# Kernel optimization log

Hardware: AMD Instinct MI355X
Metric: run time of the kernel (lower is better)

Reference implementation:

```python
import jax, jax.numpy as jnp
import numpy as np

N_HEADS = 16
ROPE_BASE = 10000.0


def rope_cos_sin(seq_len, dim, base=ROPE_BASE):
    inv_freq = 1.0 / (base ** (jnp.arange(0, dim, 2, dtype=jnp.float32) / dim))
    t = jnp.arange(seq_len, dtype=jnp.float32)
    freqs = jnp.outer(t, inv_freq)              # (S, dim/2)
    emb = jnp.concatenate([freqs, freqs], -1)   # (S, dim)
    return jnp.cos(emb), jnp.sin(emb)


def rotate_half(x):
    half = x.shape[-1] // 2
    return jnp.concatenate([-x[..., half:], x[..., :half]], axis=-1)


def setup_inputs() -> dict:
    key = jax.random.key(0)
    ks = jax.random.split(key, 6)
    B, S, D, DL, DKV = 2, 2048, 2048, 512, 2048
    s = 0.02
    return {
        "hidden_states": jax.random.normal(ks[0], (B, S, D), jnp.float32),
        "Wq": jax.random.normal(ks[1], (N_HEADS * 128, D), jnp.float32) * s,
        "Wc": jax.random.normal(ks[2], (DL, D), jnp.float32) * s,
        "Wk": jax.random.normal(ks[3], (DKV, DL), jnp.float32) * s,
        "Wv": jax.random.normal(ks[4], (DKV, DL), jnp.float32) * s,
        "Wo": jax.random.normal(ks[5], (D, N_HEADS * 128), jnp.float32) * s,
    }


def reference(hidden_states, Wq, Wc, Wk, Wv, Wo):
    B, S, D = hidden_states.shape
    H = N_HEADS
    DH = Wq.shape[0] // H

    # Q projection
    q = (hidden_states @ Wq.T).reshape(B, S, H, DH).transpose(0, 2, 1, 3)  # (B,H,S,DH)
    # latent KV compression + decompression
    c_kv = hidden_states @ Wc.T                                            # (B,S,DL)
    k = (c_kv @ Wk.T).reshape(B, S, H, DH).transpose(0, 2, 1, 3)
    v = (c_kv @ Wv.T).reshape(B, S, H, DH).transpose(0, 2, 1, 3)

    # RoPE (positions 0..S-1 for both q and k; no cache)
    cos, sin = rope_cos_sin(S, DH)
    cos = cos[None, None].astype(q.dtype)
    sin = sin[None, None].astype(q.dtype)
    q = q * cos + rotate_half(q) * sin
    k = k * cos + rotate_half(k) * sin

    scale = 1.0 / np.sqrt(DH).astype(np.float32)
    scores = jnp.einsum('bhqd,bhkd->bhqk', q, k) * scale
    causal = jnp.where(jnp.arange(S)[None, :] > jnp.arange(S)[:, None],
                       jnp.float32(-jnp.inf), jnp.float32(0.0))
    scores = scores + causal[None, None].astype(scores.dtype)
    attn = jax.nn.softmax(scores.astype(jnp.float32), axis=-1).astype(q.dtype)
    out = jnp.einsum('bhqk,bhkd->bhqd', attn, v)
    out = out.transpose(0, 2, 1, 3).reshape(B, S, H * DH)
    return out @ Wo.T
```

## Files before the change

### kernel.cpp

```cpp
#include <hip/hip_runtime.h>
#include <hip/hip_bf16.h>
#include <stdint.h>

typedef __bf16 bf16_t;
typedef __bf16 bf16x8 __attribute__((ext_vector_type(8)));
typedef float f32x4 __attribute__((ext_vector_type(4)));
typedef unsigned short u16;
typedef u16 u16x8 __attribute__((ext_vector_type(8)));
typedef u16 u16x4 __attribute__((ext_vector_type(4)));

#define AS1 __attribute__((address_space(1)))
#define AS3 __attribute__((address_space(3)))

__device__ __forceinline__ u16 f2bf(float f) {
    uint32_t u = __builtin_bit_cast(uint32_t, f);
    u += 0x7FFFu + ((u >> 16) & 1u);
    return (u16)(u >> 16);
}
__device__ __forceinline__ float bf2f(u16 h) {
    return __builtin_bit_cast(float, (uint32_t)h << 16);
}
__device__ __forceinline__ u16 f2bf_fast(float f) {
    return __builtin_bit_cast(u16, (__bf16)f);
}

__global__ void k_f32_to_bf16(const float* __restrict__ in, u16* __restrict__ out, int n4) {
    int i = blockIdx.x * blockDim.x + threadIdx.x;
    int stride = gridDim.x * blockDim.x;
    for (; i < n4; i += stride) {
        float4 v = ((const float4*)in)[i];
        ushort4 o;
        o.x = f2bf(v.x); o.y = f2bf(v.y); o.z = f2bf(v.z); o.w = f2bf(v.w);
        ((ushort4*)out)[i] = o;
    }
}

template <int OUTMODE>
__global__ __launch_bounds__(256) void k_gemm_bt(
    const u16* __restrict__ A, const u16* __restrict__ Bm,
    void* __restrict__ C, void* __restrict__ C2, int M, int N, int K)
{
    __shared__ u16 lA[128 * 32];
    __shared__ u16 lB[128 * 32];

    const int t = threadIdx.x;
    const int lane = t & 63;
    const int wave = t >> 6;
    const int wr = wave >> 1, wc = wave & 1;

    const int nwg = gridDim.x * gridDim.y;
    const int id = blockIdx.y * gridDim.x + blockIdx.x;
    const int id2 = (id & 7) * (nwg >> 3) + (id >> 3);
    const int bx = id2 % gridDim.x, by = id2 / gridDim.x;
    const int bm = by * 128, bn = bx * 128;

    const int srow = t >> 2;
    const int scol = (t & 3) * 8;
    const size_t a0 = (size_t)(bm + srow) * K + scol;
    const size_t a1 = (size_t)(bm + 64 + srow) * K + scol;
    const size_t b0 = (size_t)(bn + srow) * K + scol;
    const size_t b1 = (size_t)(bn + 64 + srow) * K + scol;

    const int fr = lane & 15;
    const int fk = (lane >> 4) * 8;

    f32x4 acc[4][4];
    const f32x4 fzero = {0.f, 0.f, 0.f, 0.f};
#pragma unroll
    for (int i = 0; i < 4; ++i)
#pragma unroll
        for (int j = 0; j < 4; ++j) acc[i][j] = fzero;

    u16* ldsA = lA + wave * 512;
    u16* ldsB = lB + wave * 512;

    for (int k0 = 0; k0 < K; k0 += 32) {
        __builtin_amdgcn_global_load_lds(
            (const AS1 void*)(A + a0 + k0), (AS3 void*)(ldsA), 16, 0, 0);
        __builtin_amdgcn_global_load_lds(
            (const AS1 void*)(A + a1 + k0), (AS3 void*)(ldsA + 2048), 16, 0, 0);
        __builtin_amdgcn_global_load_lds(
            (const AS1 void*)(Bm + b0 + k0), (AS3 void*)(ldsB), 16, 0, 0);
        __builtin_amdgcn_global_load_lds(
            (const AS1 void*)(Bm + b1 + k0), (AS3 void*)(ldsB + 2048), 16, 0, 0);
        __syncthreads();

        bf16x8 af[4], bfv[4];
#pragma unroll
        for (int mi = 0; mi < 4; ++mi)
            af[mi] = *(const bf16x8*)&lA[(wr * 64 + mi * 16 + fr) * 32 + fk];
#pragma unroll
        for (int ni = 0; ni < 4; ++ni)
            bfv[ni] = *(const bf16x8*)&lB[(wc * 64 + ni * 16 + fr) * 32 + fk];
#pragma unroll
        for (int mi = 0; mi < 4; ++mi)
#pragma unroll
            for (int ni = 0; ni < 4; ++ni)
                acc[mi][ni] = __builtin_amdgcn_mfma_f32_16x16x32_bf16(
                    af[mi], bfv[ni], acc[mi][ni], 0, 0, 0);
        __syncthreads();
    }

    const int cr = (lane >> 4) * 4;
    const int cc = lane & 15;
#pragma unroll
    for (int mi = 0; mi < 4; ++mi) {
#pragma unroll
        for (int ni = 0; ni < 4; ++ni) {
            const int row = bm + wr * 64 + mi * 16 + cr;
            const int col = bn + wc * 64 + ni * 16 + cc;
            if constexpr (OUTMODE == 1) {
#pragma unroll
                for (int r = 0; r < 4; ++r)
                    ((float*)C)[(size_t)(row + r) * N + col] = acc[mi][ni][r];
            } else if constexpr (OUTMODE == 3) {
                if (col < 2048) {
#pragma unroll
                    for (int r = 0; r < 4; ++r)
                        ((u16*)C)[(size_t)(row + r) * 2048 + col] = f2bf(acc[mi][ni][r]);
                } else {
#pragma unroll
                    for (int r = 0; r < 4; ++r)
                        ((u16*)C2)[(size_t)(row + r) * 512 + (col - 2048)] = f2bf(acc[mi][ni][r]);
                }
            } else if constexpr (OUTMODE == 4) {
                if (col < 2048) {
#pragma unroll
                    for (int r = 0; r < 4; ++r)
                        ((u16*)C)[(size_t)(row + r) * 2048 + col] = f2bf(acc[mi][ni][r]);
                } else {
                    const int c2 = col - 2048;
                    const int b = row >> 11, s0 = row & 2047;
                    const int h = c2 >> 7, d = c2 & 127;
                    u16x4 pk;
#pragma unroll
                    for (int r = 0; r < 4; ++r) pk[r] = f2bf(acc[mi][ni][r]);
                    *(u16x4*)((u16*)C2 + ((size_t)((b * 16 + h) * 128 + d)) * 2048 + s0) = pk;
                }
            }
        }
    }
}

__global__ void k_rope(u16* __restrict__ x, int S, int n) {
    int i = blockIdx.x * blockDim.x + threadIdx.x;
    if (i >= n) return;
    const int j = i & 63;
    const int h = (i >> 6) & 15;
    const int row = i >> 10;
    const int s = row & (S - 1);
    const float L2B = 13.287712379549449f;
    float inv = exp2f(-(float)(2 * j) * (L2B / 128.f));
    float ang = (float)s * inv;
    float c, sn;
    sincosf(ang, &sn, &c);
    size_t base = (size_t)row * 2048 + h * 128 + j;
    float x1 = bf2f(x[base]);
    float x2 = bf2f(x[base + 64]);
    x[base]      = f2bf(x1 * c - x2 * sn);
    x[base + 64] = f2bf(x2 * c + x1 * sn);
}

__global__ __launch_bounds__(512, 2) void k_flash_mfma(
    const u16* __restrict__ Q, const u16* __restrict__ K, const u16* __restrict__ VT,
    u16* __restrict__ O)
{
    constexpr int S = 2048, HD = 2048;
    constexpr float M0 = 8.f;
    __shared__ __align__(16) u16 K0A[32 * 128];
    __shared__ __align__(16) u16 K1A[32 * 128];
    __shared__ __align__(16) u16 K0B[32 * 128];
    __shared__ __align__(16) u16 K1B[32 * 128];
    __shared__ __align__(16) u16 V0A[128 * 32];
    __shared__ __align__(16) u16 V1A[128 * 32];
    __shared__ __align__(16) u16 V0B[128 * 32];
    __shared__ __align__(16) u16 V1B[128 * 32];
    __shared__ __align__(16) u16 Pl[8][32 * 40];
    __shared__ __align__(16) u16 MO[4][32][128];
    __shared__ float ML[4][32];

    const int t = threadIdx.x;
    const int lane = t & 63;
    const int w = t >> 6;
    const int rg = w >> 1;
    const int h = w & 1;

    const int bid = blockIdx.x;
    const int lg = (bid & 7) * 64 + (bid >> 3);
    const int c  = lg & 63;
    const int pair = (lg >> 6) * 4 + (c & 3);
    const int qt = 15 - (c >> 2);
    const int b = pair >> 4, hh = pair & 15;
    const int wq0 = qt * 128 + rg * 32;

    const u16* qg = Q + ((size_t)b * S) * HD + hh * 128;
    const u16* kg = K + ((size_t)b * S) * HD + hh * 128;
    const u16* vg = VT + ((size_t)pair) * 128 * S;

    const int r16 = lane & 15;
    const int g4 = lane >> 4;

    const float scale = 0.08838834764831845f * 1.4426950408889634f;
    bf16x8 aQ[2][4];
#pragma unroll
    for (int qi = 0; qi < 2; ++qi) {
        const u16* qr = qg + (size_t)(wq0 + qi * 16 + r16) * HD;
#pragma unroll
        for (int dk = 0; dk < 4; ++dk) {
            u16x8 u = *(const u16x8*)(qr + dk * 32 + g4 * 8);
            u16x8 uu;
#pragma unroll
            for (int j = 0; j < 8; ++j) uu[j] = f2bf(bf2f(u[j]) * scale);
            aQ[qi][dk] = __builtin_bit_cast(bf16x8, uu);
        }
    }

    f32x4 oa[2][8];
    f32x4 lP[2];
    const f32x4 fzero = {0.f, 0.f, 0.f, 0.f};
#pragma unroll
    for (int qi = 0; qi < 2; ++qi) {
        lP[qi] = fzero;
#pragma unroll
        for (int dj = 0; dj < 8; ++dj) oa[qi][dj] = fzero;
    }

    const int diag = 4 * qt + rg;
    const int tend = ((diag & 1) == h) ? diag : diag - 1;
    const int nr = 2 * qt + 2;

    auto stage = [&](u16 (&Kd0)[32 * 128], u16 (&Kd1)[32 * 128],
                     u16 (&Vd0)[128 * 32], u16 (&Vd1)[128 * 32], int j0) {
        const int off = t * 16;
        const int kv = off >> 8, c16 = (off >> 4) & 15;
        const int ck = (c16 ^ (kv & 15)) * 8;
        __builtin_amdgcn_global_load_lds(
            (const AS1 void*)(kg + (size_t)(j0 + kv) * HD + ck),
            (AS3 void*)((char*)&Kd0[0] + off), 16, 0, 0);
        __builtin_amdgcn_global_load_lds(
            (const AS1 void*)(kg + (size_t)(j0 + 32 + kv) * HD + ck),
            (AS3 void*)((char*)&Kd1[0] + off), 16, 0, 0);
        const int d = off >> 6, cv = (off >> 4) & 3;
        const int cx = (cv ^ ((d >> 1) & 3)) * 8;
        __builtin_amdgcn_global_load_lds(
            (const AS1 void*)(vg + (size_t)d * S + j0 + cx),
            (AS3 void*)((char*)&Vd0[0] + off), 16, 0, 0);
        __builtin_amdgcn_global_load_lds(
            (const AS1 void*)(vg + (size_t)d * S + j0 + 32 + cx),
            (AS3 void*)((char*)&Vd1[0] + off), 16, 0, 0);
    };

    auto compute = [&](int tix, const u16* Kc, const u16* Vc) {
        f32x4 sc[2][2];
#pragma unroll
        for (int qi = 0; qi < 2; ++qi) { sc[qi][0] = fzero; sc[qi][1] = fzero; }
#pragma unroll
        for (int dk = 0; dk < 4; ++dk) {
            const int kv0 = r16, kv1 = 16 + r16;
            bf16x8 k0 = *(const bf16x8*)((const char*)Kc +
                         kv0 * 256 + (((dk * 4 + g4) ^ (kv0 & 15)) << 4));
            bf16x8 k1 = *(const bf16x8*)((const char*)Kc +
                         kv1 * 256 + (((dk * 4 + g4) ^ (kv1 & 15)) << 4));
            sc[0][0] = __builtin_amdgcn_mfma_f32_16x16x32_bf16(aQ[0][dk], k0, sc[0][0], 0, 0, 0);
            sc[0][1] = __builtin_amdgcn_mfma_f32_16x16x32_bf16(aQ[0][dk], k1, sc[0][1], 0, 0, 0);
            sc[1][0] = __builtin_amdgcn_mfma_f32_16x16x32_bf16(aQ[1][dk], k0, sc[1][0], 0, 0, 0);
            sc[1][1] = __builtin_amdgcn_mfma_f32_16x16x32_bf16(aQ[1][dk], k1, sc[1][1], 0, 0, 0);
        }

        if (tix == diag) {
#pragma unroll
            for (int qi = 0; qi < 2; ++qi)
#pragma unroll
                for (int kf = 0; kf < 2; ++kf)
#pragma unroll
                    for (int r = 0; r < 4; ++r) {
                        const int lr = qi * 16 + g4 * 4 + r;
                        const int lc = kf * 16 + r16;
                        if (lc > lr) sc[qi][kf][r] = -1e30f;
                    }
        }

#pragma unroll
        for (int qi = 0; qi < 2; ++qi)
#pragma unroll
            for (int kf = 0; kf < 2; ++kf)
#pragma unroll
                for (int r = 0; r < 4; ++r) {
                    float pp = __builtin_amdgcn_exp2f(sc[qi][kf][r] - M0);
                    lP[qi][r] += pp;
                    Pl[w][(qi * 16 + g4 * 4 + r) * 40 + kf * 16 + r16] = f2bf_fast(pp);
                }

        bf16x8 pa[2];
#pragma unroll
        for (int qi = 0; qi < 2; ++qi)
            pa[qi] = *(const bf16x8*)&Pl[w][(qi * 16 + r16) * 40 + g4 * 8];
#pragma unroll
        for (int dj = 0; dj < 8; ++dj) {
            const int d = dj * 16 + r16;
            bf16x8 bV = *(const bf16x8*)((const char*)Vc +
                         d * 64 + ((g4 ^ ((d >> 1) & 3)) << 4));
            oa[0][dj] = __builtin_amdgcn_mfma_f32_16x16x32_bf16(pa[0], bV, oa[0][dj], 0, 0, 0);
            oa[1][dj] = __builtin_amdgcn_mfma_f32_16x16x32_bf16(pa[1], bV, oa[1][dj], 0, 0, 0);
        }
    };

    const u16* myKA = h ? &K1A[0] : &K0A[0];
    const u16* myVA = h ? &V1A[0] : &V0A[0];
    const u16* myKB = h ? &K1B[0] : &K0B[0];
    const u16* myVB = h ? &V1B[0] : &V0B[0];

    stage(K0A, K1A, V0A, V1A, 0);
    __syncthreads();
    for (int j = 0; j < nr; j += 2) {
        if (j + 1 < nr) stage(K0B, K1B, V0B, V1B, (j + 1) * 64);
        { const int tix = 2 * j + h; if (tix <= tend) compute(tix, myKA, myVA); }
        __syncthreads();
        if (j + 2 < nr) stage(K0A, K1A, V0A, V1A, (j + 2) * 64);
        { const int tix = 2 * (j + 1) + h; if (tix <= tend) compute(tix, myKB, myVB); }
        __syncthreads();
    }

#pragma unroll
    for (int qi = 0; qi < 2; ++qi)
#pragma unroll
        for (int r = 0; r < 4; ++r) {
            float v = lP[qi][r];
            v += __shfl_xor(v, 1);
            v += __shfl_xor(v, 2);
            v += __shfl_xor(v, 4);
            v += __shfl_xor(v, 8);
            lP[qi][r] = v;
        }

    if (h) {
#pragma unroll
        for (int qi = 0; qi < 2; ++qi)
#pragma unroll
            for (int r = 0; r < 4; ++r) {
                const int row = qi * 16 + g4 * 4 + r;
                ML[rg][row] = lP[qi][r];
#pragma unroll
                for (int dj = 0; dj < 8; ++dj)
                    MO[rg][row][dj * 16 + r16] = f2bf_fast(oa[qi][dj][r]);
            }
    }
    __syncthreads();
    if (!h) {
#pragma unroll
        for (int qi = 0; qi < 2; ++qi) {
#pragma unroll
            for (int r = 0; r < 4; ++r) {
                const int row = qi * 16 + g4 * 4 + r;
                const float inv = 1.f / (lP[qi][r] + ML[rg][row]);
                u16* orow = O + (size_t)(b * S + wq0 + row) * HD + hh * 128;
#pragma unroll
                for (int dj = 0; dj < 8; ++dj) {
                    const float o2 = bf2f(MO[rg][row][dj * 16 + r16]);
                    orow[dj * 16 + r16] = f2bf((oa[qi][dj][r] + o2) * inv);
                }
            }
        }
    }
}

extern "C" void kernel_launch(void* const* d_in, const int* in_sizes, int n_in,
                              void* d_out, int out_size, void* d_ws, size_t ws_size,
                              hipStream_t stream) {
    const float* hs = (const float*)d_in[0];
    const float* Wq = (const float*)d_in[1];
    const float* Wc = (const float*)d_in[2];
    const float* Wk = (const float*)d_in[3];
    const float* Wv = (const float*)d_in[4];
    const float* Wo = (const float*)d_in[5];

    const int B = 2, S = 2048, D = 2048, DL = 512, H = 16;
    const int M = B * S;

    char* p = (char*)d_ws;
    u16* hs_bf   = (u16*)p; p += (size_t)M * D * 2;
    u16* WqWc_bf = (u16*)p; p += (size_t)(D + DL) * D * 2;
    u16* WkWv_bf = (u16*)p; p += (size_t)(2 * D) * DL * 2;
    u16* Wo_bf   = (u16*)p; p += (size_t)D * D * 2;
    u16* qb      = (u16*)p; p += (size_t)M * D * 2;
    u16* kb      = (u16*)p; p += (size_t)M * D * 2;
    u16* vbT     = (u16*)p; p += (size_t)M * D * 2;
    u16* ckv     = (u16*)p; p += (size_t)M * DL * 2;
    u16* attn    = (u16*)p; p += (size_t)M * D * 2;

    auto conv = [&](const float* in, u16* out, size_t n) {
        int n4 = (int)(n / 4);
        int blocks = (n4 + 255) / 256;
        if (blocks > 4096) blocks = 4096;
        k_f32_to_bf16<<<blocks, 256, 0, stream>>>(in, out, n4);
    };
    conv(hs, hs_bf, (size_t)M * D);
    conv(Wq, WqWc_bf, (size_t)D * D);
    conv(Wc, WqWc_bf + (size_t)D * D, (size_t)DL * D);
    conv(Wk, WkWv_bf, (size_t)D * DL);
    conv(Wv, WkWv_bf + (size_t)D * DL, (size_t)D * DL);
    conv(Wo, Wo_bf, (size_t)D * D);

    k_gemm_bt<3><<<dim3((D + DL) / 128, M / 128), 256, 0, stream>>>(
        hs_bf, WqWc_bf, qb, ckv, M, D + DL, D);
    k_gemm_bt<4><<<dim3((2 * D) / 128, M / 128), 256, 0, stream>>>(
        ckv, WkWv_bf, kb, vbT, M, 2 * D, DL);

    {
        int n = M * H * 64;
        int blocks = (n + 255) / 256;
        k_rope<<<blocks, 256, 0, stream>>>(qb, S, n);
        k_rope<<<blocks, 256, 0, stream>>>(kb, S, n);
    }

    k_flash_mfma<<<512, 512, 0, stream>>>(qb, kb, vbT, attn);

    k_gemm_bt<1><<<dim3(D / 128, M / 128), 256, 0, stream>>>(
        attn, Wo_bf, (float*)d_out, nullptr, M, D, D);
}
```

Measured before the change: 264.4 us.

## Double-buffer GEMM LDS tiles with K=64 steps and XOR-swizzled layout

The bf16 GEMM kernel now uses two LDS buffers per operand with a K-step of 64. The next tile is loaded asynchronously via global_load_lds while MFMAs run on the current one, and there is one barrier per stage instead of two. An XOR swizzle on the 16-byte column chunks is meant to avoid LDS bank conflicts, and launch bounds request 2 workgroups per CU. LDS use grows to 64KB per block, which may limit occupancy. The loop also assumes K is a multiple of 128 and has no wait on the async loads beyond the barrier.

```diff
diff --git a/kernel.cpp b/kernel.cpp
--- a/kernel.cpp
+++ b/kernel.cpp
@@ -36,12 +36,14 @@
 }
 
 template <int OUTMODE>
-__global__ __launch_bounds__(256) void k_gemm_bt(
+__global__ __launch_bounds__(256, 2) void k_gemm_bt(
     const u16* __restrict__ A, const u16* __restrict__ Bm,
     void* __restrict__ C, void* __restrict__ C2, int M, int N, int K)
 {
-    __shared__ u16 lA[128 * 32];
-    __shared__ u16 lB[128 * 32];
+    __shared__ __align__(16) u16 sA0[128 * 64];
+    __shared__ __align__(16) u16 sA1[128 * 64];
+    __shared__ __align__(16) u16 sB0[128 * 64];
+    __shared__ __align__(16) u16 sB1[128 * 64];
 
     const int t = threadIdx.x;
     const int lane = t & 63;
@@ -54,15 +56,13 @@
     const int bx = id2 % gridDim.x, by = id2 / gridDim.x;
     const int bm = by * 128, bn = bx * 128;
 
-    const int srow = t >> 2;
-    const int scol = (t & 3) * 8;
-    const size_t a0 = (size_t)(bm + srow) * K + scol;
-    const size_t a1 = (size_t)(bm + 64 + srow) * K + scol;
-    const size_t b0 = (size_t)(bn + srow) * K + scol;
-    const size_t b1 = (size_t)(bn + 64 + srow) * K + scol;
+    const int srow0 = t >> 3;
+    const int scol = ((t & 7) ^ (srow0 & 7)) * 8;
+    const size_t aBase = (size_t)(bm + srow0) * K + scol;
+    const size_t bBase = (size_t)(bn + srow0) * K + scol;
 
     const int fr = lane & 15;
-    const int fk = (lane >> 4) * 8;
+    const int g4 = lane >> 4;
 
     f32x4 acc[4][4];
     const f32x4 fzero = {0.f, 0.f, 0.f, 0.f};
@@ -71,33 +71,54 @@
 #pragma unroll
         for (int j = 0; j < 4; ++j) acc[i][j] = fzero;
 
-    u16* ldsA = lA + wave * 512;
-    u16* ldsB = lB + wave * 512;
-
-    for (int k0 = 0; k0 < K; k0 += 32) {
-        __builtin_amdgcn_global_load_lds(
-            (const AS1 void*)(A + a0 + k0), (AS3 void*)(ldsA), 16, 0, 0);
-        __builtin_amdgcn_global_load_lds(
-            (const AS1 void*)(A + a1 + k0), (AS3 void*)(ldsA + 2048), 16, 0, 0);
-        __builtin_amdgcn_global_load_lds(
-            (const AS1 void*)(Bm + b0 + k0), (AS3 void*)(ldsB), 16, 0, 0);
-        __builtin_amdgcn_global_load_lds(
-            (const AS1 void*)(Bm + b1 + k0), (AS3 void*)(ldsB + 2048), 16, 0, 0);
+    auto stage = [&](u16 (&dA)[128 * 64], u16 (&dB)[128 * 64], int k0) {
+#pragma unroll
+        for (int i = 0; i < 4; ++i) {
+            __builtin_amdgcn_global_load_lds(
+                (const AS1 void*)(A + aBase + (size_t)i * 32 * K + k0),
+                (AS3 void*)((char*)&dA[0] + i * 4096 + t * 16), 16, 0, 0);
+            __builtin_amdgcn_global_load_lds(
+                (const AS1 void*)(Bm + bBase + (size_t)i * 32 * K + k0),
+                (AS3 void*)((char*)&dB[0] + i * 4096 + t * 16), 16, 0, 0);
+        }
+    };
+
+    auto compute = [&](const u16 (&sA)[128 * 64], const u16 (&sB)[128 * 64]) {
+        bf16x8 af[4][2], bfv[4][2];
+#pragma unroll
+        for (int mi = 0; mi < 4; ++mi) {
+            const int row = wr * 64 + mi * 16 + fr;
+            const char* rp = (const char*)&sA[0] + row * 128;
+#pragma unroll
+            for (int kk = 0; kk < 2; ++kk)
+                af[mi][kk] = *(const bf16x8*)(rp + (((kk * 4 + g4) ^ (row & 7)) << 4));
+        }
+#pragma unroll
+        for (int ni = 0; ni < 4; ++ni) {
+            const int row = wc * 64 + ni * 16 + fr;
+            const char* rp = (const char*)&sB[0] + row * 128;
+#pragma unroll
+            for (int kk = 0; kk < 2; ++kk)
+                bfv[ni][kk] = *(const bf16x8*)(rp + (((kk * 4 + g4) ^ (row & 7)) << 4));
+        }
+#pragma unroll
+        for (int kk = 0; kk < 2; ++kk)
+#pragma unroll
+            for (int mi = 0; mi < 4; ++mi)
+#pragma unroll
+                for (int ni = 0; ni < 4; ++ni)
+                    acc[mi][ni] = __builtin_amdgcn_mfma_f32_16x16x32_bf16(
+                        af[mi][kk], bfv[ni][kk], acc[mi][ni], 0, 0, 0);
+    };
+
+    stage(sA0, sB0, 0);
+    __syncthreads();
+    for (int k0 = 0; k0 < K; k0 += 128) {
+        if (k0 + 64 < K) stage(sA1, sB1, k0 + 64);
+        compute(sA0, sB0);
         __syncthreads();
-
-        bf16x8 af[4], bfv[4];
-#pragma unroll
-        for (int mi = 0; mi < 4; ++mi)
-            af[mi] = *(const bf16x8*)&lA[(wr * 64 + mi * 16 + fr) * 32 + fk];
-#pragma unroll
-        for (int ni = 0; ni < 4; ++ni)
-            bfv[ni] = *(const bf16x8*)&lB[(wc * 64 + ni * 16 + fr) * 32 + fk];
-#pragma unroll
-        for (int mi = 0; mi < 4; ++mi)
-#pragma unroll
-            for (int ni = 0; ni < 4; ++ni)
-                acc[mi][ni] = __builtin_amdgcn_mfma_f32_16x16x32_bf16(
-                    af[mi], bfv[ni], acc[mi][ni], 0, 0, 0);
+        if (k0 + 128 < K) stage(sA0, sB0, k0 + 128);
+        compute(sA1, sB1);
         __syncthreads();
     }
 
```

Result: faster. 231.1 us (-12.6%).
